# Kernel tuning notes

Hardware: AMD Instinct MI355X
Metric: run time of the kernel (lower is better)

The kernel has to match this reference:

```python
import jax, jax.numpy as jnp
import numpy as np

B, K, N, E, D = 32, 32, 2048, 16384, 768
L_GNN, L_TR, H = 2, 4, 12
FF, VOCAB, N_ROLES, MAX_POS, N_HOPS = 3072, 25, 2, 64, 16


def setup_inputs() -> dict:
    key = jax.random.key(0)
    ks = jax.random.split(key, 32)
    s = 0.02
    inp = {
        "raw_features": jax.random.normal(ks[0], (B, K, D), jnp.float32),
        "x0": jax.random.randint(ks[1], (K, N), 0, VOCAB),
        "edge0": jax.random.randint(ks[2], (K, 2, E), 0, N),
        "batch0": jnp.sort(jax.random.randint(ks[3], (K, N), 0, B), axis=-1),
        "x1": jax.random.randint(ks[4], (K, N), 0, VOCAB),
        "edge1": jax.random.randint(ks[5], (K, 2, E), 0, N),
        "batch1": jnp.sort(jax.random.randint(ks[6], (K, N), 0, B), axis=-1),
        "role_ids": jax.random.randint(ks[7], (B, K), 0, N_ROLES),
        "position_ids": jax.random.randint(ks[8], (B, K), 0, MAX_POS),
        "hop_ids": jax.random.randint(ks[9], (B, K), 0, N_HOPS),
        # GNNForProtein params (shared across slots and both proteins)
        "amino_embed": jax.random.normal(ks[10], (VOCAB, D)) * s,
        "gnn_W": jax.random.normal(ks[11], (L_GNN, D, D)) * s,
        "gnn_b": jnp.zeros((L_GNN, D)),
        # GraphBert embeddings
        "role_emb": jax.random.normal(ks[12], (N_ROLES, D)) * s,
        "pos_emb": jax.random.normal(ks[13], (MAX_POS, D)) * s,
        "hop_emb": jax.random.normal(ks[14], (N_HOPS, D)) * s,
        "emb_ln_scale": jnp.ones((D,)),
        "emb_ln_bias": jnp.zeros((D,)),
        # GraphBert transformer layers (stacked over L_TR)
        "Wq": jax.random.normal(ks[15], (L_TR, D, D)) * s,
        "bq": jnp.zeros((L_TR, D)),
        "Wk": jax.random.normal(ks[16], (L_TR, D, D)) * s,
        "bk": jnp.zeros((L_TR, D)),
        "Wv": jax.random.normal(ks[17], (L_TR, D, D)) * s,
        "bv": jnp.zeros((L_TR, D)),
        "Wo": jax.random.normal(ks[18], (L_TR, D, D)) * s,
        "bo": jnp.zeros((L_TR, D)),
        "ln1_s": jnp.ones((L_TR, D)),
        "ln1_b": jnp.zeros((L_TR, D)),
        "W1": jax.random.normal(ks[19], (L_TR, D, FF)) * s,
        "b1": jnp.zeros((L_TR, FF)),
        "W2": jax.random.normal(ks[20], (L_TR, FF, D)) * s,
        "b2": jnp.zeros((L_TR, D)),
        "ln2_s": jnp.ones((L_TR, D)),
        "ln2_b": jnp.zeros((L_TR, D)),
    }
    return inp


def _ln(x, s, b):
    m = jnp.mean(x, -1, keepdims=True)
    v = jnp.mean(jnp.square(x - m), -1, keepdims=True)
    return (x - m) * jax.lax.rsqrt(v + 1e-12) * s + b


def _gnn(node_ids, edges, batch_idx, amino_embed, W, b):
    # One protein slot: GCN message passing + mean readout per graph in batch.
    h = amino_embed[node_ids]                      # [N, D]
    src, dst = edges[0], edges[1]
    for l in range(W.shape[0]):
        agg = jax.ops.segment_sum(h[src], dst, num_segments=N)
        h = jax.nn.relu((h + agg) @ W[l] + b[l])
    sums = jax.ops.segment_sum(h, batch_idx, num_segments=B)
    cnt = jax.ops.segment_sum(jnp.ones((h.shape[0], 1), h.dtype), batch_idx, num_segments=B)
    return sums / jnp.maximum(cnt, 1.0)           # [B, D]


def reference(raw_features, x0, edge0, batch0, x1, edge1, batch1, role_ids, position_ids, hop_ids,
              amino_embed, gnn_W, gnn_b, role_emb, pos_emb, hop_emb, emb_ln_scale, emb_ln_bias,
              Wq, bq, Wk, bk, Wv, bv, Wo, bo, ln1_s, ln1_b, W1, b1, W2, b2, ln2_s, ln2_b):
    # vmap over the K protein slots replaces the original Python loop (same math).
    gnn_v = jax.vmap(_gnn, in_axes=(0, 0, 0, None, None, None))
    p0 = gnn_v(x0, edge0, batch0, amino_embed, gnn_W, gnn_b)   # [K, B, D]
    p1 = gnn_v(x1, edge1, batch1, amino_embed, gnn_W, gnn_b)   # [K, B, D]
    feats = raw_features + jnp.transpose(p0 + p1, (1, 0, 2))   # [B, K, D]
    # GraphBert embeddings + encoder
    h = feats + role_emb[role_ids] + pos_emb[position_ids] + hop_emb[hop_ids]
    h = _ln(h, emb_ln_scale, emb_ln_bias)
    dh = D // H
    scale = float(1.0 / np.sqrt(dh))
    for l in range(Wq.shape[0]):
        q = (h @ Wq[l] + bq[l]).reshape(B, K, H, dh)
        kk = (h @ Wk[l] + bk[l]).reshape(B, K, H, dh)
        v = (h @ Wv[l] + bv[l]).reshape(B, K, H, dh)
        att = jax.nn.softmax(jnp.einsum('bqhd,bkhd->bhqk', q, kk) * scale, axis=-1)
        ctx = jnp.einsum('bhqk,bkhd->bqhd', att, v).reshape(B, K, D)
        h = _ln(h + ctx @ Wo[l] + bo[l], ln1_s[l], ln1_b[l])
        f = jax.nn.gelu(h @ W1[l] + b1[l]) @ W2[l] + b2[l]
        h = _ln(h + f, ln2_s[l], ln2_b[l])
    return h
```

## Files before the change

kernel.cpp:

```cpp
#include <hip/hip_runtime.h>
#include <hip/hip_bf16.h>
#include <math.h>

using bf16 = __hip_bfloat16;
typedef __attribute__((ext_vector_type(8))) short short8;
typedef __attribute__((ext_vector_type(4))) float floatx4;
typedef __attribute__((ext_vector_type(4))) short short4v;

#define NB   32
#define NK   32
#define NNODE 2048
#define NEDGE 16384
#define ND   768
#define NHH  12
#define DHH  64
#define NFF  3072
#define NG   64
#define LTR  4
#define VOCAB 25

static __device__ __forceinline__ float b2f(bf16 x) { return __bfloat162float(x); }
static __device__ __forceinline__ bf16 f2b(float x) { return __float2bfloat16(x); }
static __device__ __forceinline__ float bs2f(short s) {
    unsigned u = ((unsigned)(unsigned short)s) << 16;
    float f; __builtin_memcpy(&f, &u, 4); return f;
}
static __device__ __forceinline__ short f2bs(float x) {
    bf16 h = f2b(x); short s; __builtin_memcpy(&s, &h, 2); return s;
}

static __device__ __forceinline__ void load_lds16(const bf16* g, bf16* l) {
    __builtin_amdgcn_global_load_lds((const __attribute__((address_space(1))) void*)g,
                                     (__attribute__((address_space(3))) void*)l, 16, 0, 0);
}

static __device__ __forceinline__ float ldf(const void* p, size_t i, bool f32) {
    return f32 ? ((const float*)p)[i] : b2f(((const bf16*)p)[i]);
}

__global__ void detect_dtype_kernel(const void* __restrict__ eln_s, int* __restrict__ flag) {
    if (threadIdx.x == 0 && blockIdx.x == 0) {
        unsigned w = ((const unsigned*)eln_s)[0];
        flag[0] = (w == 0x3F800000u) ? 1 : 0;
    }
}

__device__ __forceinline__ void conv_tile(const void* __restrict__ src, size_t srcOff,
                                          bf16* __restrict__ dst, int R, int Cn,
                                          int tr, int tc, bool f32, int t,
                                          short (*tile)[70]) {
    int r0 = tr * 64, c0 = tc * 64;
    int rr = t >> 4, c4 = (t & 15) * 4;
    #pragma unroll
    for (int p = 0; p < 4; ++p) {
        int r = rr + p * 16;
        size_t base = srcOff + (size_t)(r0 + r) * Cn + c0 + c4;
        short4v s;
        if (f32) {
            float4 v = *(const float4*)((const float*)src + base);
            s.x = f2bs(v.x); s.y = f2bs(v.y); s.z = f2bs(v.z); s.w = f2bs(v.w);
        } else {
            s = *(const short4v*)((const short*)src + base);
        }
        tile[r][c4]     = s.x; tile[r][c4 + 1] = s.y;
        tile[r][c4 + 2] = s.z; tile[r][c4 + 3] = s.w;
    }
    __syncthreads();
    #pragma unroll
    for (int p = 0; p < 4; ++p) {
        int c = rr + p * 16;
        short4v o;
        o.x = tile[c4][c];     o.y = tile[c4 + 1][c];
        o.z = tile[c4 + 2][c]; o.w = tile[c4 + 3][c];
        *(short4v*)((short*)dst + (size_t)(c0 + c) * R + r0 + c4) = o;
    }
}

__global__ __launch_bounds__(256) void convert_gnn_kernel(const void* __restrict__ gnnW,
                                                          bf16* __restrict__ gnnT,
                                                          const int* __restrict__ flag) {
    __shared__ short tile[64][70];
    bool f32 = flag[0] != 0;
    int bid = blockIdx.x;
    int id = bid / 144, tl = bid % 144;
    conv_tile(gnnW, (size_t)id * 589824, gnnT + (size_t)id * 589824,
              768, 768, tl / 12, tl % 12, f32, threadIdx.x, tile);
}

__global__ __launch_bounds__(256) void convert_layer_kernel(
    const void* __restrict__ Wq, const void* __restrict__ Wk, const void* __restrict__ Wv,
    const void* __restrict__ Wo, const void* __restrict__ W1, const void* __restrict__ W2,
    int l, bf16* __restrict__ qkvT, bf16* __restrict__ oT,
    bf16* __restrict__ w1T, bf16* __restrict__ w2T, const int* __restrict__ flag) {
    __shared__ short tile[64][70];
    bool f32 = flag[0] != 0;
    int bid = blockIdx.x, t = threadIdx.x;
    if (bid < 432) {
        int m = bid / 144, tl = bid % 144;
        const void* src = (m == 0) ? Wq : ((m == 1) ? Wk : Wv);
        conv_tile(src, (size_t)l * 589824, qkvT + (size_t)m * 589824,
                  768, 768, tl / 12, tl % 12, f32, t, tile);
    } else if (bid < 576) {
        int tl = bid - 432;
        conv_tile(Wo, (size_t)l * 589824, oT, 768, 768, tl / 12, tl % 12, f32, t, tile);
    } else if (bid < 1152) {
        int tl = bid - 576;
        conv_tile(W1, (size_t)l * 768 * 3072, w1T, 768, 3072, tl / 48, tl % 48, f32, t, tile);
    } else {
        int tl = bid - 1152;
        conv_tile(W2, (size_t)l * 3072 * 768, w2T, 3072, 768, tl / 12, tl % 12, f32, t, tile);
    }
}

__global__ __launch_bounds__(256) void pack_bias_kernel(
    const void* __restrict__ gnnb, const void* __restrict__ bq, const void* __restrict__ bk,
    const void* __restrict__ bv, const void* __restrict__ bo, const void* __restrict__ b1,
    const void* __restrict__ b2, float* __restrict__ out, const int* __restrict__ flag) {
    bool f32 = flag[0] != 0;
    int i = blockIdx.x * 256 + threadIdx.x;
    if (i >= 1536 + LTR * 6912) return;
    float v;
    if (i < 1536) v = ldf(gnnb, i, f32);
    else {
        int j = i - 1536, l = j / 6912, r = j % 6912;
        if      (r <  768) v = ldf(bq, l * 768 + r, f32);
        else if (r < 1536) v = ldf(bk, l * 768 + r - 768, f32);
        else if (r < 2304) v = ldf(bv, l * 768 + r - 1536, f32);
        else if (r < 3072) v = ldf(bo, l * 768 + r - 2304, f32);
        else if (r < 6144) v = ldf(b1, l * 3072 + r - 3072, f32);
        else               v = ldf(b2, l * 768 + r - 6144, f32);
    }
    out[i] = v;
}

__global__ __launch_bounds__(192) void e1_kernel(const void* __restrict__ emb,
                                                 const bf16* __restrict__ w0T,
                                                 bf16* __restrict__ E1,
                                                 const int* __restrict__ flag) {
    bool f32 = flag[0] != 0;
    int v = blockIdx.x, t = threadIdx.x;
    float acc[4] = {0.f, 0.f, 0.f, 0.f};
    for (int k = 0; k < ND; k += 4) {
        float e0 = ldf(emb, (size_t)v * ND + k,     f32);
        float e1 = ldf(emb, (size_t)v * ND + k + 1, f32);
        float e2 = ldf(emb, (size_t)v * ND + k + 2, f32);
        float e3 = ldf(emb, (size_t)v * ND + k + 3, f32);
        #pragma unroll
        for (int j = 0; j < 4; ++j) {
            const short4v w = *(const short4v*)&w0T[(size_t)(t * 4 + j) * ND + k];
            acc[j] += e0 * bs2f(w.x) + e1 * bs2f(w.y) + e2 * bs2f(w.z) + e3 * bs2f(w.w);
        }
    }
    short4v o; o.x = f2bs(acc[0]); o.y = f2bs(acc[1]); o.z = f2bs(acc[2]); o.w = f2bs(acc[3]);
    ((short4v*)(E1 + (size_t)v * ND))[t] = o;
}

__global__ __launch_bounds__(256) void count_deg_kernel(const int* __restrict__ edge0,
                                                        const int* __restrict__ edge1,
                                                        int* __restrict__ deg) {
    int gid = blockIdx.x;
    int g = gid >> 6, chunk = gid & 63;
    const int* ep = (g < NK) ? (edge0 + (size_t)g * 2 * NEDGE)
                             : (edge1 + (size_t)(g - NK) * 2 * NEDGE);
    int e = chunk * 256 + threadIdx.x;
    int dst = ep[NEDGE + e];
    atomicAdd(&deg[g * NNODE + dst], 1);
}

__global__ __launch_bounds__(256) void scan_deg_kernel(int* __restrict__ deg,
                                                       int* __restrict__ indptr) {
    int g = blockIdx.x, t = threadIdx.x;
    __shared__ int sums[256];
    int loc[8]; int s = 0;
    #pragma unroll
    for (int i = 0; i < 8; ++i) { loc[i] = deg[g * NNODE + t * 8 + i]; s += loc[i]; }
    sums[t] = s; __syncthreads();
    for (int off = 1; off < 256; off <<= 1) {
        int v = (t >= off) ? sums[t - off] : 0;
        __syncthreads();
        sums[t] += v;
        __syncthreads();
    }
    int run = sums[t] - s;
    #pragma unroll
    for (int i = 0; i < 8; ++i) {
        indptr[g * (NNODE + 1) + t * 8 + i] = run;
        deg[g * NNODE + t * 8 + i] = run;
        run += loc[i];
    }
    if (t == 255) indptr[g * (NNODE + 1) + NNODE] = run;
}

__global__ __launch_bounds__(256) void fill_csr_kernel(const int* __restrict__ edge0,
                                                       const int* __restrict__ edge1,
                                                       int* __restrict__ cursor,
                                                       int* __restrict__ csr_src) {
    int gid = blockIdx.x;
    int g = gid >> 6, chunk = gid & 63;
    const int* ep = (g < NK) ? (edge0 + (size_t)g * 2 * NEDGE)
                             : (edge1 + (size_t)(g - NK) * 2 * NEDGE);
    int e = chunk * 256 + threadIdx.x;
    int src = ep[e];
    int dst = ep[NEDGE + e];
    int p = atomicAdd(&cursor[g * NNODE + dst], 1);
    csr_src[(size_t)g * NEDGE + p] = src;
}

__global__ __launch_bounds__(64) void batch_count_kernel(const int* __restrict__ batch0,
                                                         const int* __restrict__ batch1,
                                                         int* __restrict__ cnt) {
    int g = blockIdx.x;
    int b = threadIdx.x;
    if (b >= NB) return;
    const int* bp = (g < NK) ? (batch0 + (size_t)g * NNODE)
                             : (batch1 + (size_t)(g - NK) * NNODE);
    int lo = 0, hi = NNODE;
    while (lo < hi) { int mid = (lo + hi) >> 1; if (bp[mid] < b) lo = mid + 1; else hi = mid; }
    int start = lo;
    hi = NNODE;
    while (lo < hi) { int mid = (lo + hi) >> 1; if (bp[mid] < b + 1) lo = mid + 1; else hi = mid; }
    cnt[g * NB + b] = lo - start;
}

__global__ __launch_bounds__(192) void gnn_layer1_kernel(const int* __restrict__ x0,
                                                         const int* __restrict__ x1,
                                                         const bf16* __restrict__ E1,
                                                         const float* __restrict__ b0,
                                                         const int* __restrict__ indptr,
                                                         const int* __restrict__ csr_src,
                                                         bf16* __restrict__ hC, int g0) {
    int id = blockIdx.x;
    int r = id & 7, q = id >> 3;
    int gl = r + 8 * (q >> 10);
    int np = q & 1023;
    int t = threadIdx.x;
    int j = t / 96, ln = t % 96;
    int n = np * 2 + j;
    int g = g0 + gl;
    const int* xg = (g < NK) ? (x0 + (size_t)g * NNODE) : (x1 + (size_t)(g - NK) * NNODE);
    int beg = indptr[g * (NNODE + 1) + n];
    int end = indptr[g * (NNODE + 1) + n + 1];
    const int* cs = csr_src + (size_t)g * NEDGE;
    const short8* E = (const short8*)E1;
    short8 v = E[(size_t)xg[n] * 96 + ln];
    float a[8];
    #pragma unroll
    for (int u = 0; u < 8; ++u) a[u] = bs2f(v[u]);
    int e = beg;
    for (; e + 3 < end; e += 4) {
        int s1 = cs[e], s2 = cs[e + 1], s3 = cs[e + 2], s4 = cs[e + 3];
        short8 w1 = E[(size_t)xg[s1] * 96 + ln];
        short8 w2 = E[(size_t)xg[s2] * 96 + ln];
        short8 w3 = E[(size_t)xg[s3] * 96 + ln];
        short8 w4 = E[(size_t)xg[s4] * 96 + ln];
        #pragma unroll
        for (int u = 0; u < 8; ++u)
            a[u] += (bs2f(w1[u]) + bs2f(w2[u])) + (bs2f(w3[u]) + bs2f(w4[u]));
    }
    for (; e < end; ++e) {
        short8 w = E[(size_t)xg[cs[e]] * 96 + ln];
        #pragma unroll
        for (int u = 0; u < 8; ++u) a[u] += bs2f(w[u]);
    }
    float4 ba = ((const float4*)b0)[ln * 2];
    float4 bb = ((const float4*)b0)[ln * 2 + 1];
    short8 o;
    o[0] = f2bs(fmaxf(a[0] + ba.x, 0.f)); o[1] = f2bs(fmaxf(a[1] + ba.y, 0.f));
    o[2] = f2bs(fmaxf(a[2] + ba.z, 0.f)); o[3] = f2bs(fmaxf(a[3] + ba.w, 0.f));
    o[4] = f2bs(fmaxf(a[4] + bb.x, 0.f)); o[5] = f2bs(fmaxf(a[5] + bb.y, 0.f));
    o[6] = f2bs(fmaxf(a[6] + bb.z, 0.f)); o[7] = f2bs(fmaxf(a[7] + bb.w, 0.f));
    ((short8*)(hC + ((size_t)gl * NNODE + n) * ND))[ln] = o;
}

__global__ __launch_bounds__(192) void gnn_aggregate_kernel(const bf16* __restrict__ hC,
                                                            const int* __restrict__ indptr,
                                                            const int* __restrict__ csr_src,
                                                            bf16* __restrict__ xC, int g0) {
    int id = blockIdx.x;
    int r = id & 7, q = id >> 3;
    int gl = r + 8 * (q >> 10);
    int np = q & 1023;
    int t = threadIdx.x;
    int j = t / 96, ln = t % 96;
    int n = np * 2 + j;
    int g = g0 + gl;
    int beg = indptr[g * (NNODE + 1) + n];
    int end = indptr[g * (NNODE + 1) + n + 1];
    const short8* hg = (const short8*)(hC + (size_t)gl * NNODE * ND);
    const int* cs = csr_src + (size_t)g * NEDGE;
    short8 v = hg[(size_t)n * 96 + ln];
    float a[8];
    #pragma unroll
    for (int u = 0; u < 8; ++u) a[u] = bs2f(v[u]);
    int e = beg;
    for (; e + 3 < end; e += 4) {
        int s1 = cs[e], s2 = cs[e + 1], s3 = cs[e + 2], s4 = cs[e + 3];
        short8 w1 = hg[(size_t)s1 * 96 + ln];
        short8 w2 = hg[(size_t)s2 * 96 + ln];
        short8 w3 = hg[(size_t)s3 * 96 + ln];
        short8 w4 = hg[(size_t)s4 * 96 + ln];
        #pragma unroll
        for (int u = 0; u < 8; ++u)
            a[u] += (bs2f(w1[u]) + bs2f(w2[u])) + (bs2f(w3[u]) + bs2f(w4[u]));
    }
    for (; e < end; ++e) {
        short8 w = hg[(size_t)cs[e] * 96 + ln];
        #pragma unroll
        for (int u = 0; u < 8; ++u) a[u] += bs2f(w[u]);
    }
    short8 o;
    #pragma unroll
    for (int u = 0; u < 8; ++u) o[u] = f2bs(a[u]);
    ((short8*)(xC + ((size_t)gl * NNODE + n) * ND))[ln] = o;
}

__global__ __launch_bounds__(512) void gemm8_pool(const bf16* __restrict__ A,
                                                  const bf16* __restrict__ BT,
                                                  const float* __restrict__ bias,
                                                  int M, int K, int N,
                                                  const int* __restrict__ batAp,
                                                  const int* __restrict__ batBp,
                                                  float* __restrict__ pool, int g0) {
    __shared__ bf16 sA[3][256][64];
    __shared__ bf16 sB[2][128][64];
    const int nt = K >> 6;
    int nTN = N >> 7;
    int xcd = blockIdx.x & 7, jb = blockIdx.x >> 3;
    int brow = (jb / nTN) * 8 + xcd;
    int bcol = jb % nTN;
    const int row0 = brow << 8, col0 = bcol << 7;
    int t = threadIdx.x;
    int wid = t >> 6, lane = t & 63;
    int wr = wid >> 1, wc = wid & 1;
    int l15 = lane & 15, kx = lane >> 4, sw = lane & 7;

    const bf16* Abase = A + (size_t)row0 * K;
    const bf16* Bbase = BT + (size_t)col0 * K;

    auto stage = [&](const bf16* g, bf16* slot, int r0) {
        int r = r0 + (t >> 3);
        int ks = ((t & 7) ^ ((t >> 3) & 7)) << 3;
        load_lds16(g + (size_t)r * K + ks, slot + ((size_t)r0 << 6) + ((size_t)t << 3));
    };
    auto rdA = [&](int s, int i, int kh) {
        return *(const short8*)&sA[s][wr * 64 + i * 16 + l15][(((kh << 2) | kx) ^ sw) << 3];
    };
    auto rdB = [&](int s, int j, int kh) {
        return *(const short8*)&sB[s][wc * 64 + j * 16 + l15][(((kh << 2) | kx) ^ sw) << 3];
    };

    stage(Abase, &sA[0][0][0], 0);   stage(Abase, &sA[0][0][0], 64);
    stage(Abase, &sA[0][0][0], 128); stage(Abase, &sA[0][0][0], 192);
    stage(Bbase, &sB[0][0][0], 0);   stage(Bbase, &sB[0][0][0], 64);
    const bf16* gA1 = Abase + 64;
    stage(gA1, &sA[1][0][0], 0);   stage(gA1, &sA[1][0][0], 64);
    stage(gA1, &sA[1][0][0], 128); stage(gA1, &sA[1][0][0], 192);
    asm volatile("s_waitcnt vmcnt(4)" ::: "memory");
    __builtin_amdgcn_s_barrier();

    floatx4 acc[4][4] = {};
    for (int kt = 0; kt < nt; ++kt) {
        int sa = kt % 3, sb = kt & 1;
        bf16* saN = &sA[(kt + 2) % 3][0][0];
        const bf16* gA = Abase + (kt + 2) * 64;
        short8 af[4], bf[4];
        #pragma unroll
        for (int i = 0; i < 4; ++i) af[i] = rdA(sa, i, 0);
        #pragma unroll
        for (int j = 0; j < 4; ++j) bf[j] = rdB(sb, j, 0);
        if (kt + 1 < nt) {
            const bf16* gB = Bbase + (kt + 1) * 64;
            bf16* sbN = &sB[(kt + 1) & 1][0][0];
            stage(gB, sbN, 0); stage(gB, sbN, 64);
        }
        if (kt + 2 < nt) { stage(gA, saN, 0); stage(gA, saN, 64); }
        __builtin_amdgcn_s_barrier();
        asm volatile("s_waitcnt lgkmcnt(0)" ::: "memory");
        __builtin_amdgcn_s_setprio(1);
        #pragma unroll
        for (int i = 0; i < 4; ++i)
            #pragma unroll
            for (int j = 0; j < 4; ++j)
                acc[i][j] = __builtin_amdgcn_mfma_f32_16x16x32_bf16(af[i], bf[j], acc[i][j], 0, 0, 0);
        __builtin_amdgcn_s_setprio(0);
        __builtin_amdgcn_s_barrier();
        #pragma unroll
        for (int i = 0; i < 4; ++i) af[i] = rdA(sa, i, 1);
        #pragma unroll
        for (int j = 0; j < 4; ++j) bf[j] = rdB(sb, j, 1);
        if (kt + 2 < nt) { stage(gA, saN, 128); stage(gA, saN, 192); }
        __builtin_amdgcn_s_barrier();
        asm volatile("s_waitcnt lgkmcnt(0)" ::: "memory");
        __builtin_amdgcn_s_setprio(1);
        #pragma unroll
        for (int i = 0; i < 4; ++i)
            #pragma unroll
            for (int j = 0; j < 4; ++j)
                acc[i][j] = __builtin_amdgcn_mfma_f32_16x16x32_bf16(af[i], bf[j], acc[i][j], 0, 0, 0);
        __builtin_amdgcn_s_setprio(0);
        if (kt + 1 < nt) {
            if (kt + 2 < nt) asm volatile("s_waitcnt vmcnt(4)" ::: "memory");
            else             asm volatile("s_waitcnt vmcnt(0)" ::: "memory");
            __builtin_amdgcn_s_barrier();
        }
    }

    __syncthreads();
    int g = g0 + (row0 >> 11);
    const int* bp = (g < NK) ? (batAp + (size_t)g * NNODE)
                             : (batBp + (size_t)(g - NK) * NNODE);
    int nbase = row0 & (NNODE - 1);
    float* pg = pool + (size_t)g * NB * ND;
    int cb = wc * 64 + l15;
    float bv[4];
    #pragma unroll
    for (int j = 0; j < 4; ++j) bv[j] = bias[col0 + cb + j * 16];
    float* lp = (float*)sA;
    int bLo = bp[nbase], bHi = bp[nbase + 255];
    int nb = (bHi - bLo + 1) * 128;
    for (int idx = t; idx < nb; idx += 512) lp[idx] = 0.f;
    __syncthreads();
    float sums[4] = {0.f, 0.f, 0.f, 0.f};
    int curb = -1;
    #pragma unroll
    for (int i = 0; i < 4; ++i) {
        int rr = nbase + wr * 64 + i * 16 + kx * 4;
        #pragma unroll
        for (int r = 0; r < 4; ++r) {
            int b = bp[rr + r];
            if (b != curb) {
                if (curb >= 0) {
                    #pragma unroll
                    for (int j = 0; j < 4; ++j)
                        atomicAdd(&lp[(curb - bLo) * 128 + cb + j * 16], sums[j]);
                }
                curb = b;
                sums[0] = sums[1] = sums[2] = sums[3] = 0.f;
            }
            #pragma unroll
            for (int j = 0; j < 4; ++j)
                sums[j] += fmaxf(acc[i][j][r] + bv[j], 0.f);
        }
    }
    #pragma unroll
    for (int j = 0; j < 4; ++j)
        atomicAdd(&lp[(curb - bLo) * 128 + cb + j * 16], sums[j]);
    __syncthreads();
    for (int idx = t; idx < nb; idx += 512) {
        float v = lp[idx];
        if (v != 0.f)
            atomicAdd(&pg[(size_t)(bLo + (idx >> 7)) * ND + col0 + (idx & 127)], v);
    }
}

__global__ __launch_bounds__(256) void gemm_tn_sk(const bf16* __restrict__ A,
                                                  const bf16* __restrict__ BT,
                                                  const float* __restrict__ bias,
                                                  void* __restrict__ C,
                                                  int M, int K, int N, int splitK,
                                                  int act, int store) {
    __shared__ bf16 lA[2][64][64];
    __shared__ bf16 lB[2][128][64];
    int nTN = N >> 7, nTM = M >> 6;
    int tiles = nTM * nTN;
    int split = blockIdx.x / tiles;
    int jt = blockIdx.x % tiles;
    int brow = jt / nTN, bcol = jt % nTN;
    int t = threadIdx.x;
    int wave = t >> 6, lane = t & 63;
    int wr = wave >> 1, wc = wave & 1;
    int l15 = lane & 15, kx = lane >> 4, sw = lane & 7;
    const int row0 = brow << 6, col0 = bcol << 7;
    const int kLen = K / splitK, kBeg = split * kLen;
    const int nt = kLen >> 6;
    const bf16* Abase = A + (size_t)row0 * K + kBeg;
    const bf16* Bbase = BT + (size_t)col0 * K + kBeg;

    auto stage = [&](const bf16* gsrc, bf16* slot, int r0) {
        int rr = r0 + (t >> 3);
        int ks = ((t & 7) ^ (rr & 7)) << 3;
        load_lds16(gsrc + (size_t)rr * K + ks, slot + ((size_t)r0 << 6) + ((size_t)t << 3));
    };
    auto stageTile = [&](int kt, int buf) {
        const bf16* gA = Abase + kt * 64;
        const bf16* gB = Bbase + kt * 64;
        stage(gA, &lA[buf][0][0], 0);  stage(gA, &lA[buf][0][0], 32);
        stage(gB, &lB[buf][0][0], 0);  stage(gB, &lB[buf][0][0], 32);
        stage(gB, &lB[buf][0][0], 64); stage(gB, &lB[buf][0][0], 96);
    };
    auto rdA = [&](int s, int i, int kh) {
        return *(const short8*)&lA[s][wr * 32 + i * 16 + l15][(((kh << 2) | kx) ^ sw) << 3];
    };
    auto rdB = [&](int s, int jj, int kh) {
        return *(const short8*)&lB[s][wc * 64 + jj * 16 + l15][(((kh << 2) | kx) ^ sw) << 3];
    };

    stageTile(0, 0);
    __syncthreads();

    floatx4 acc[2][4] = {};
    int cur = 0;
    for (int kt = 0; kt < nt; ++kt) {
        if (kt + 1 < nt) stageTile(kt + 1, cur ^ 1);
        #pragma unroll
        for (int kh = 0; kh < 2; ++kh) {
            short8 af[2], bf2[4];
            #pragma unroll
            for (int i = 0; i < 2; ++i) af[i] = rdA(cur, i, kh);
            #pragma unroll
            for (int jj = 0; jj < 4; ++jj) bf2[jj] = rdB(cur, jj, kh);
            #pragma unroll
            for (int i = 0; i < 2; ++i)
                #pragma unroll
                for (int jj = 0; jj < 4; ++jj)
                    acc[i][jj] = __builtin_amdgcn_mfma_f32_16x16x32_bf16(af[i], bf2[jj], acc[i][jj], 0, 0, 0);
        }
        __syncthreads();
        cur ^= 1;
    }
    #pragma unroll
    for (int i = 0; i < 2; ++i) {
        int rbase = row0 + wr * 32 + i * 16 + kx * 4;
        #pragma unroll
        for (int j = 0; j < 4; ++j) {
            int c = col0 + wc * 64 + j * 16 + l15;
            float bv = (split == 0) ? bias[c] : 0.f;
            #pragma unroll
            for (int r = 0; r < 4; ++r) {
                float v = acc[i][j][r] + bv;
                if (act == 1) v = fmaxf(v, 0.f);
                else if (act == 2) {
                    float x = v;
                    float u = 1.5957691216057308f * (x + 0.044715f * x * x * x);
                    v = x / (1.f + __expf(-u));
                }
                size_t idx = (size_t)(rbase + r) * N + c;
                if (store == 0)      atomicAdd(&((float*)C)[idx], v);
                else if (store == 1) ((float*)C)[idx] = v;
                else                 ((bf16*)C)[idx] = f2b(v);
            }
        }
    }
}

__device__ __forceinline__ float block_sum_768(float v, int t, float* red) {
    #pragma unroll
    for (int off = 32; off > 0; off >>= 1) v += __shfl_xor(v, off);
    if ((t & 63) == 0) red[t >> 6] = v;
    __syncthreads();
    float s = red[0] + red[1] + red[2] + red[3];
    __syncthreads();
    return s;
}

__device__ __forceinline__ void block_ln_768(float (&x)[3], int t,
                                             const void* __restrict__ s,
                                             const void* __restrict__ b,
                                             size_t sOff, bool f32,
                                             float (&y)[3], float* red) {
    float mean = block_sum_768(x[0] + x[1] + x[2], t, red) * (1.f / 768.f);
    float vs = 0.f;
    #pragma unroll
    for (int e = 0; e < 3; ++e) { float d = x[e] - mean; vs += d * d; }
    float var = block_sum_768(vs, t, red) * (1.f / 768.f);
    float inv = rsqrtf(var + 1e-12f);
    #pragma unroll
    for (int e = 0; e < 3; ++e) {
        int d = t + e * 256;
        y[e] = (x[e] - mean) * inv * ldf(s, sOff + d, f32) + ldf(b, sOff + d, f32);
    }
}

__global__ __launch_bounds__(256) void combine_embed_ln_kernel(
    const void* __restrict__ raw, const float* __restrict__ pooled,
    const int* __restrict__ cnt,
    const int* __restrict__ role_ids, const int* __restrict__ pos_ids, const int* __restrict__ hop_ids,
    const void* __restrict__ role_emb, const void* __restrict__ pos_emb, const void* __restrict__ hop_emb,
    const void* __restrict__ lns, const void* __restrict__ lnb,
    float* __restrict__ hT, bf16* __restrict__ hbf,
    const int* __restrict__ flag) {
    bool f32 = flag[0] != 0;
    __shared__ float red[8];
    int token = blockIdx.x;
    int b = token >> 5, k = token & 31;
    int t = threadIdx.x;
    int rid = role_ids[b * NK + k];
    int pid = pos_ids[b * NK + k];
    int hid = hop_ids[b * NK + k];
    float inv0 = 1.f / (float)max(cnt[k * NB + b], 1);
    float inv1 = 1.f / (float)max(cnt[(NK + k) * NB + b], 1);
    float x[3], y[3];
    #pragma unroll
    for (int e = 0; e < 3; ++e) {
        int d = t + e * 256;
        float p0 = pooled[((size_t)k * NB + b) * ND + d] * inv0;
        float p1 = pooled[((size_t)(NK + k) * NB + b) * ND + d] * inv1;
        x[e] = ldf(raw, (size_t)token * ND + d, f32) + p0 + p1
             + ldf(role_emb, (size_t)rid * ND + d, f32)
             + ldf(pos_emb, (size_t)pid * ND + d, f32)
             + ldf(hop_emb, (size_t)hid * ND + d, f32);
    }
    block_ln_768(x, t, lns, lnb, 0, f32, y, red);
    #pragma unroll
    for (int e = 0; e < 3; ++e) {
        int d = t + e * 256;
        hT[(size_t)token * ND + d] = y[e];
        hbf[(size_t)token * ND + d] = f2b(y[e]);
    }
}

__global__ __launch_bounds__(256) void add_ln_kernel(float* __restrict__ hT,
                                                     const void* __restrict__ lns,
                                                     const void* __restrict__ lnb,
                                                     unsigned long long sOff,
                                                     void* __restrict__ outp, int extOut,
                                                     const int* __restrict__ flag) {
    bool f32 = flag[0] != 0;
    __shared__ float red[8];
    int token = blockIdx.x;
    int t = threadIdx.x;
    float x[3], y[3];
    #pragma unroll
    for (int e = 0; e < 3; ++e) {
        int d = t + e * 256;
        x[e] = hT[(size_t)token * ND + d];
    }
    block_ln_768(x, t, lns, lnb, sOff, f32, y, red);
    #pragma unroll
    for (int e = 0; e < 3; ++e) {
        int d = t + e * 256;
        size_t idx = (size_t)token * ND + d;
        hT[idx] = y[e];
        if (extOut && f32) ((float*)outp)[idx] = y[e];
        else               ((bf16*)outp)[idx] = f2b(y[e]);
    }
}

__global__ __launch_bounds__(256) void attn_kernel(const bf16* __restrict__ qkv,
                                                   bf16* __restrict__ ctx) {
    int blk = blockIdx.x;
    int b = blk / NHH, h = blk % NHH;
    __shared__ float lq[NK][DHH], lk[NK][DHH], lv[NK][DHH];
    __shared__ float ls[NK][NK];
    int t = threadIdx.x;
    {
        int tok = t >> 3, d8 = (t & 7) * 8;
        size_t base = ((size_t)(b * NK + tok)) * (3 * ND) + h * DHH + d8;
        short8 q8 = *(const short8*)&qkv[base];
        short8 k8 = *(const short8*)&qkv[base + ND];
        short8 v8 = *(const short8*)&qkv[base + 2 * ND];
        #pragma unroll
        for (int j = 0; j < 8; ++j) {
            lq[tok][d8 + j] = bs2f(q8[j]);
            lk[tok][d8 + j] = bs2f(k8[j]);
            lv[tok][d8 + j] = bs2f(v8[j]);
        }
    }
    __syncthreads();
    const float scale = 0.125f;
    for (int i = t; i < NK * NK; i += 256) {
        int qi = i >> 5, kj = i & 31;
        float s = 0.f;
        #pragma unroll
        for (int d = 0; d < DHH; ++d) s += lq[qi][d] * lk[kj][d];
        ls[qi][kj] = s * scale;
    }
    __syncthreads();
    if (t < NK) {
        float m = -1e30f;
        for (int j = 0; j < NK; ++j) m = fmaxf(m, ls[t][j]);
        float sum = 0.f;
        for (int j = 0; j < NK; ++j) { float e = expf(ls[t][j] - m); ls[t][j] = e; sum += e; }
        float inv = 1.f / sum;
        for (int j = 0; j < NK; ++j) ls[t][j] *= inv;
    }
    __syncthreads();
    for (int i = t; i < NK * DHH; i += 256) {
        int qi = i >> 6, d = i & 63;
        float s = 0.f;
        #pragma unroll
        for (int j = 0; j < NK; ++j) s += ls[qi][j] * lv[j][d];
        ctx[((size_t)(b * NK + qi)) * ND + h * DHH + d] = f2b(s);
    }
}

extern "C" void kernel_launch(void* const* d_in, const int* in_sizes, int n_in,
                              void* d_out, int out_size, void* d_ws, size_t ws_size,
                              hipStream_t stream) {
    const void* raw      = d_in[0];
    const int*  x0       = (const int*)d_in[1];
    const int*  edge0    = (const int*)d_in[2];
    const int*  batch0   = (const int*)d_in[3];
    const int*  x1       = (const int*)d_in[4];
    const int*  edge1    = (const int*)d_in[5];
    const int*  batch1   = (const int*)d_in[6];
    const int*  role_ids = (const int*)d_in[7];
    const int*  pos_ids  = (const int*)d_in[8];
    const int*  hop_ids  = (const int*)d_in[9];
    const void* amino    = d_in[10];
    const void* gnnW     = d_in[11];
    const void* gnnb     = d_in[12];
    const void* role_emb = d_in[13];
    const void* pos_emb  = d_in[14];
    const void* hop_emb  = d_in[15];
    const void* eln_s    = d_in[16];
    const void* eln_b    = d_in[17];
    const void* Wq       = d_in[18];
    const void* bq       = d_in[19];
    const void* Wk       = d_in[20];
    const void* bk       = d_in[21];
    const void* Wv       = d_in[22];
    const void* bv       = d_in[23];
    const void* Wo       = d_in[24];
    const void* bo       = d_in[25];
    const void* ln1_s    = d_in[26];
    const void* ln1_b    = d_in[27];
    const void* W1       = d_in[28];
    const void* b1       = d_in[29];
    const void* W2       = d_in[30];
    const void* b2       = d_in[31];
    const void* ln2_s    = d_in[32];
    const void* ln2_b    = d_in[33];

    char* ws = (char*)d_ws;
    size_t off = 0;
    auto alloc = [&](size_t bytes) -> void* {
        void* p = ws + off;
        off = (off + bytes + 255) & ~(size_t)255;
        return p;
    };
    int*   dflag   = (int*)alloc(256);
    float* pooled  = (float*)alloc((size_t)NG * NB * ND * 4);
    int*   cntb    = (int*)alloc((size_t)NG * NB * 4);
    int*   indptr  = (int*)alloc((size_t)NG * (NNODE + 1) * 4);
    int*   csr_src = (int*)alloc((size_t)NG * NEDGE * 4);
    int*   degcur  = (int*)alloc((size_t)NG * NNODE * 4);
    bf16*  gnnT    = (bf16*)alloc((size_t)2 * ND * ND * 2);
    bf16*  E1      = (bf16*)alloc((size_t)VOCAB * ND * 2);
    float* biasPk  = (float*)alloc((size_t)(1536 + LTR * 6912) * 4);
    const size_t QS = (size_t)3 * ND * ND, OS = (size_t)ND * ND;
    const size_t S1 = (size_t)ND * NFF,    S2 = (size_t)NFF * ND;
    bf16*  qkvT    = (bf16*)alloc(QS * 2);
    bf16*  oT      = (bf16*)alloc(OS * 2);
    bf16*  w1T     = (bf16*)alloc(S1 * 2);
    bf16*  w2T     = (bf16*)alloc(S2 * 2);

    const size_t perG  = (size_t)NNODE * ND * 2;
    const size_t bigTR = 21 * 1024 * 1024;
    int gc = 8;
    for (int cand = 32; cand >= 8; cand >>= 1) {
        size_t bigGNN = 2 * (size_t)cand * perG;
        size_t need = off + (bigGNN > bigTR ? bigGNN : bigTR) + (1 << 20);
        if (need <= ws_size) { gc = cand; break; }
    }
    char* bigbase = (char*)alloc(2 * (size_t)gc * perG > bigTR ? 2 * (size_t)gc * perG : bigTR);
    bf16* hC = (bf16*)bigbase;
    bf16* xC = (bf16*)(bigbase + (size_t)gc * perG);
    size_t toff = 0;
    auto talloc = [&](size_t bytes) -> void* {
        void* p = bigbase + toff;
        toff = (toff + bytes + 255) & ~(size_t)255;
        return p;
    };
    float* hT    = (float*)talloc((size_t)NB * NK * ND * 4);
    bf16*  hbf   = (bf16*)talloc((size_t)NB * NK * ND * 2);
    bf16*  qkvb  = (bf16*)talloc((size_t)NB * NK * 3 * ND * 2);
    bf16*  ctxb  = (bf16*)talloc((size_t)NB * NK * ND * 2);
    bf16*  ffbuf = (bf16*)talloc((size_t)NB * NK * NFF * 2);

    auto gemm_sk = [&](const bf16* A, const bf16* BT, const float* bias, void* C,
                       int Mm, int Kk, int Nn, int splitK, int act, int store) {
        int blocks = (Mm >> 6) * (Nn >> 7) * splitK;
        gemm_tn_sk<<<blocks, 256, 0, stream>>>(A, BT, bias, C, Mm, Kk, Nn, splitK, act, store);
    };

    detect_dtype_kernel<<<1, 64, 0, stream>>>(eln_s, dflag);

    convert_gnn_kernel<<<288, 256, 0, stream>>>(gnnW, gnnT, dflag);
    pack_bias_kernel<<<(1536 + LTR * 6912 + 255) / 256, 256, 0, stream>>>(
        gnnb, bq, bk, bv, bo, b1, b2, biasPk, dflag);
    e1_kernel<<<VOCAB, 192, 0, stream>>>(amino, gnnT, E1, dflag);

    hipMemsetAsync(degcur, 0, (size_t)NG * NNODE * 4, stream);
    hipMemsetAsync(pooled, 0, (size_t)NG * NB * ND * 4, stream);
    count_deg_kernel<<<NG * 64, 256, 0, stream>>>(edge0, edge1, degcur);
    scan_deg_kernel<<<NG, 256, 0, stream>>>(degcur, indptr);
    fill_csr_kernel<<<NG * 64, 256, 0, stream>>>(edge0, edge1, degcur, csr_src);
    batch_count_kernel<<<NG, 64, 0, stream>>>(batch0, batch1, cntb);

    for (int g0 = 0; g0 < NG; g0 += gc) {
        gnn_layer1_kernel<<<gc * (NNODE / 2), 192, 0, stream>>>(x0, x1, E1, biasPk,
                                                                indptr, csr_src, hC, g0);
        gnn_aggregate_kernel<<<gc * (NNODE / 2), 192, 0, stream>>>(hC, indptr, csr_src, xC, g0);
        int blocks = ((gc * NNODE) >> 8) * (ND >> 7);
        gemm8_pool<<<blocks, 512, 0, stream>>>(xC, gnnT + (size_t)ND * ND, biasPk + ND,
                                               gc * NNODE, ND, ND,
                                               batch0, batch1, pooled, g0);
    }

    combine_embed_ln_kernel<<<NB * NK, 256, 0, stream>>>(
        raw, pooled, cntb, role_ids, pos_ids, hop_ids,
        role_emb, pos_emb, hop_emb, eln_s, eln_b, hT, hbf, dflag);

    const int M = NB * NK;
    for (int l = 0; l < LTR; ++l) {
        convert_layer_kernel<<<1728, 256, 0, stream>>>(Wq, Wk, Wv, Wo, W1, W2, l,
                                                       qkvT, oT, w1T, w2T, dflag);
        const float* lb = biasPk + 1536 + l * 6912;
        gemm_sk(hbf, qkvT, lb, qkvb, M, ND, 3 * ND, 1, 0, 2);
        attn_kernel<<<NB * NHH, 256, 0, stream>>>(qkvb, ctxb);
        gemm_sk(ctxb, oT, lb + 2304, hT, M, ND, ND, 2, 0, 0);
        add_ln_kernel<<<M, 256, 0, stream>>>(hT, ln1_s, ln1_b,
                                             (unsigned long long)l * ND, hbf, 0, dflag);
        gemm_sk(hbf, w1T, lb + 3072, ffbuf, M, ND, NFF, 1, 2, 2);
        gemm_sk(ffbuf, w2T, lb + 6144, hT, M, NFF, ND, 4, 0, 0);
        int ext = (l == LTR - 1) ? 1 : 0;
        void* outb = ext ? d_out : (void*)hbf;
        add_ln_kernel<<<M, 256, 0, stream>>>(hT, ln2_s, ln2_b,
                                             (unsigned long long)l * ND, outb, ext, dflag);
    }
}
```

Baseline: 1.257 ms.

## Batch weight conversion, vectorize CSR build, read first GNN weight directly

Converts all four transformer layers' weights in one launch when workspace allows, replacing four per-layer conversion launches. The first GNN layer's embedding projection now reads the original weights directly, so only the second GNN weight gets transposed. Degree counting and CSR fill each process four edges per thread with vector loads, and workspace selection now prefers a larger GNN chunk size (64 graphs per pass). The Wo GEMM split-K changes from 2 to 3, and the upfront conversion uses more workspace memory.

After: 1.364 ms. 8.5% more time.

```diff
diff --git a/kernel.cpp b/kernel.cpp
--- a/kernel.cpp
+++ b/kernel.cpp
@@ -81,20 +81,16 @@
                                                           const int* __restrict__ flag) {
     __shared__ short tile[64][70];
     bool f32 = flag[0] != 0;
-    int bid = blockIdx.x;
-    int id = bid / 144, tl = bid % 144;
-    conv_tile(gnnW, (size_t)id * 589824, gnnT + (size_t)id * 589824,
+    int tl = blockIdx.x;
+    conv_tile(gnnW, (size_t)589824, gnnT,
               768, 768, tl / 12, tl % 12, f32, threadIdx.x, tile);
 }
 
-__global__ __launch_bounds__(256) void convert_layer_kernel(
-    const void* __restrict__ Wq, const void* __restrict__ Wk, const void* __restrict__ Wv,
-    const void* __restrict__ Wo, const void* __restrict__ W1, const void* __restrict__ W2,
-    int l, bf16* __restrict__ qkvT, bf16* __restrict__ oT,
-    bf16* __restrict__ w1T, bf16* __restrict__ w2T, const int* __restrict__ flag) {
-    __shared__ short tile[64][70];
-    bool f32 = flag[0] != 0;
-    int bid = blockIdx.x, t = threadIdx.x;
+__device__ __forceinline__ void conv_layer_body(
+    const void* Wq, const void* Wk, const void* Wv, const void* Wo,
+    const void* W1, const void* W2, int l,
+    bf16* qkvT, bf16* oT, bf16* w1T, bf16* w2T,
+    bool f32, int bid, int t, short (*tile)[70]) {
     if (bid < 432) {
         int m = bid / 144, tl = bid % 144;
         const void* src = (m == 0) ? Wq : ((m == 1) ? Wk : Wv);
@@ -110,6 +106,29 @@
         int tl = bid - 1152;
         conv_tile(W2, (size_t)l * 3072 * 768, w2T, 3072, 768, tl / 12, tl % 12, f32, t, tile);
     }
+}
+
+__global__ __launch_bounds__(256) void convert_layer_kernel(
+    const void* __restrict__ Wq, const void* __restrict__ Wk, const void* __restrict__ Wv,
+    const void* __restrict__ Wo, const void* __restrict__ W1, const void* __restrict__ W2,
+    int l, bf16* __restrict__ qkvT, bf16* __restrict__ oT,
+    bf16* __restrict__ w1T, bf16* __restrict__ w2T, const int* __restrict__ flag) {
+    __shared__ short tile[64][70];
+    conv_layer_body(Wq, Wk, Wv, Wo, W1, W2, l, qkvT, oT, w1T, w2T,
+                    flag[0] != 0, blockIdx.x, threadIdx.x, tile);
+}
+
+__global__ __launch_bounds__(256) void convert_layers_all(
+    const void* __restrict__ Wq, const void* __restrict__ Wk, const void* __restrict__ Wv,
+    const void* __restrict__ Wo, const void* __restrict__ W1, const void* __restrict__ W2,
+    bf16* __restrict__ qkvT, bf16* __restrict__ oT,
+    bf16* __restrict__ w1T, bf16* __restrict__ w2T, const int* __restrict__ flag) {
+    __shared__ short tile[64][70];
+    int l = blockIdx.x / 1728, bid = blockIdx.x % 1728;
+    conv_layer_body(Wq, Wk, Wv, Wo, W1, W2, l,
+                    qkvT + (size_t)l * 3 * ND * ND, oT + (size_t)l * ND * ND,
+                    w1T + (size_t)l * ND * NFF, w2T + (size_t)l * NFF * ND,
+                    flag[0] != 0, bid, threadIdx.x, tile);
 }
 
 __global__ __launch_bounds__(256) void pack_bias_kernel(
@@ -134,21 +153,21 @@
 }
 
 __global__ __launch_bounds__(192) void e1_kernel(const void* __restrict__ emb,
-                                                 const bf16* __restrict__ w0T,
+                                                 const void* __restrict__ gnnW,
                                                  bf16* __restrict__ E1,
                                                  const int* __restrict__ flag) {
     bool f32 = flag[0] != 0;
     int v = blockIdx.x, t = threadIdx.x;
     float acc[4] = {0.f, 0.f, 0.f, 0.f};
-    for (int k = 0; k < ND; k += 4) {
-        float e0 = ldf(emb, (size_t)v * ND + k,     f32);
-        float e1 = ldf(emb, (size_t)v * ND + k + 1, f32);
-        float e2 = ldf(emb, (size_t)v * ND + k + 2, f32);
-        float e3 = ldf(emb, (size_t)v * ND + k + 3, f32);
-        #pragma unroll
-        for (int j = 0; j < 4; ++j) {
-            const short4v w = *(const short4v*)&w0T[(size_t)(t * 4 + j) * ND + k];
-            acc[j] += e0 * bs2f(w.x) + e1 * bs2f(w.y) + e2 * bs2f(w.z) + e3 * bs2f(w.w);
+    for (int k = 0; k < ND; ++k) {
+        float e = ldf(emb, (size_t)v * ND + k, f32);
+        if (f32) {
+            float4 w = *(const float4*)((const float*)gnnW + (size_t)k * ND + t * 4);
+            acc[0] += e * w.x; acc[1] += e * w.y; acc[2] += e * w.z; acc[3] += e * w.w;
+        } else {
+            short4v w = *(const short4v*)((const short*)gnnW + (size_t)k * ND + t * 4);
+            acc[0] += e * bs2f(w.x); acc[1] += e * bs2f(w.y);
+            acc[2] += e * bs2f(w.z); acc[3] += e * bs2f(w.w);
         }
     }
     short4v o; o.x = f2bs(acc[0]); o.y = f2bs(acc[1]); o.z = f2bs(acc[2]); o.w = f2bs(acc[3]);
@@ -159,12 +178,15 @@
                                                         const int* __restrict__ edge1,
                                                         int* __restrict__ deg) {
     int gid = blockIdx.x;
-    int g = gid >> 6, chunk = gid & 63;
+    int g = gid >> 4, chunk = gid & 15;
     const int* ep = (g < NK) ? (edge0 + (size_t)g * 2 * NEDGE)
                              : (edge1 + (size_t)(g - NK) * 2 * NEDGE);
-    int e = chunk * 256 + threadIdx.x;
-    int dst = ep[NEDGE + e];
-    atomicAdd(&deg[g * NNODE + dst], 1);
+    int base = (chunk * 256 + threadIdx.x) * 4;
+    int4 d = *(const int4*)&ep[NEDGE + base];
+    atomicAdd(&deg[g * NNODE + d.x], 1);
+    atomicAdd(&deg[g * NNODE + d.y], 1);
+    atomicAdd(&deg[g * NNODE + d.z], 1);
+    atomicAdd(&deg[g * NNODE + d.w], 1);
 }
 
 __global__ __launch_bounds__(256) void scan_deg_kernel(int* __restrict__ deg,
@@ -196,14 +218,19 @@
                                                        int* __restrict__ cursor,
                                                        int* __restrict__ csr_src) {
     int gid = blockIdx.x;
-    int g = gid >> 6, chunk = gid & 63;
+    int g = gid >> 4, chunk = gid & 15;
     const int* ep = (g < NK) ? (edge0 + (size_t)g * 2 * NEDGE)
                              : (edge1 + (size_t)(g - NK) * 2 * NEDGE);
-    int e = chunk * 256 + threadIdx.x;
-    int src = ep[e];
-    int dst = ep[NEDGE + e];
-    int p = atomicAdd(&cursor[g * NNODE + dst], 1);
-    csr_src[(size_t)g * NEDGE + p] = src;
+    int base = (chunk * 256 + threadIdx.x) * 4;
+    int4 sv = *(const int4*)&ep[base];
+    int4 dv = *(const int4*)&ep[NEDGE + base];
+    int* cur = cursor + g * NNODE;
+    int* cg = (int*)(csr_src + (size_t)g * NEDGE);
+    int p;
+    p = atomicAdd(&cur[dv.x], 1); cg[p] = sv.x;
+    p = atomicAdd(&cur[dv.y], 1); cg[p] = sv.y;
+    p = atomicAdd(&cur[dv.z], 1); cg[p] = sv.z;
+    p = atomicAdd(&cur[dv.w], 1); cg[p] = sv.w;
 }
 
 __global__ __launch_bounds__(64) void batch_count_kernel(const int* __restrict__ batch0,
@@ -735,24 +762,31 @@
     int*   indptr  = (int*)alloc((size_t)NG * (NNODE + 1) * 4);
     int*   csr_src = (int*)alloc((size_t)NG * NEDGE * 4);
     int*   degcur  = (int*)alloc((size_t)NG * NNODE * 4);
-    bf16*  gnnT    = (bf16*)alloc((size_t)2 * ND * ND * 2);
+    bf16*  gnnT    = (bf16*)alloc((size_t)ND * ND * 2);
     bf16*  E1      = (bf16*)alloc((size_t)VOCAB * ND * 2);
     float* biasPk  = (float*)alloc((size_t)(1536 + LTR * 6912) * 4);
     const size_t QS = (size_t)3 * ND * ND, OS = (size_t)ND * ND;
     const size_t S1 = (size_t)ND * NFF,    S2 = (size_t)NFF * ND;
-    bf16*  qkvT    = (bf16*)alloc(QS * 2);
-    bf16*  oT      = (bf16*)alloc(OS * 2);
-    bf16*  w1T     = (bf16*)alloc(S1 * 2);
-    bf16*  w2T     = (bf16*)alloc(S2 * 2);
+    const size_t wPerLayer = (QS + OS + S1 + S2) * 2;
 
     const size_t perG  = (size_t)NNODE * ND * 2;
     const size_t bigTR = 21 * 1024 * 1024;
-    int gc = 8;
-    for (int cand = 32; cand >= 8; cand >>= 1) {
-        size_t bigGNN = 2 * (size_t)cand * perG;
-        size_t need = off + (bigGNN > bigTR ? bigGNN : bigTR) + (1 << 20);
-        if (need <= ws_size) { gc = cand; break; }
-    }
+    int gc = 8, nlw = 1;
+    {
+        const int cands[6][2] = {{64, 4}, {64, 1}, {32, 4}, {32, 1}, {16, 1}, {8, 1}};
+        for (int i = 0; i < 6; ++i) {
+            size_t bigGNN = 2 * (size_t)cands[i][0] * perG;
+            size_t big = bigGNN > bigTR ? bigGNN : bigTR;
+            if (off + (size_t)cands[i][1] * wPerLayer + big + (1 << 20) <= ws_size) {
+                gc = cands[i][0]; nlw = cands[i][1]; break;
+            }
+        }
+    }
+    bf16* qkvT = (bf16*)alloc(QS * 2 * nlw);
+    bf16* oT   = (bf16*)alloc(OS * 2 * nlw);
+    bf16* w1T  = (bf16*)alloc(S1 * 2 * nlw);
+    bf16* w2T  = (bf16*)alloc(S2 * 2 * nlw);
+
     char* bigbase = (char*)alloc(2 * (size_t)gc * perG > bigTR ? 2 * (size_t)gc * perG : bigTR);
     bf16* hC = (bf16*)bigbase;
     bf16* xC = (bf16*)(bigbase + (size_t)gc * perG);
@@ -776,16 +810,19 @@
 
     detect_dtype_kernel<<<1, 64, 0, stream>>>(eln_s, dflag);
 
-    convert_gnn_kernel<<<288, 256, 0, stream>>>(gnnW, gnnT, dflag);
+    convert_gnn_kernel<<<144, 256, 0, stream>>>(gnnW, gnnT, dflag);
     pack_bias_kernel<<<(1536 + LTR * 6912 + 255) / 256, 256, 0, stream>>>(
         gnnb, bq, bk, bv, bo, b1, b2, biasPk, dflag);
-    e1_kernel<<<VOCAB, 192, 0, stream>>>(amino, gnnT, E1, dflag);
+    e1_kernel<<<VOCAB, 192, 0, stream>>>(amino, gnnW, E1, dflag);
+    if (nlw == 4)
+        convert_layers_all<<<4 * 1728, 256, 0, stream>>>(Wq, Wk, Wv, Wo, W1, W2,
+                                                         qkvT, oT, w1T, w2T, dflag);
 
     hipMemsetAsync(degcur, 0, (size_t)NG * NNODE * 4, stream);
     hipMemsetAsync(pooled, 0, (size_t)NG * NB * ND * 4, stream);
-    count_deg_kernel<<<NG * 64, 256, 0, stream>>>(edge0, edge1, degcur);
+    count_deg_kernel<<<NG * 16, 256, 0, stream>>>(edge0, edge1, degcur);
     scan_deg_kernel<<<NG, 256, 0, stream>>>(degcur, indptr);
-    fill_csr_kernel<<<NG * 64, 256, 0, stream>>>(edge0, edge1, degcur, csr_src);
+    fill_csr_kernel<<<NG * 16, 256, 0, stream>>>(edge0, edge1, degcur, csr_src);
     batch_count_kernel<<<NG, 64, 0, stream>>>(batch0, batch1, cntb);
 
     for (int g0 = 0; g0 < NG; g0 += gc) {
@@ -793,7 +830,7 @@
                                                                 indptr, csr_src, hC, g0);
         gnn_aggregate_kernel<<<gc * (NNODE / 2), 192, 0, stream>>>(hC, indptr, csr_src, xC, g0);
         int blocks = ((gc * NNODE) >> 8) * (ND >> 7);
-        gemm8_pool<<<blocks, 512, 0, stream>>>(xC, gnnT + (size_t)ND * ND, biasPk + ND,
+        gemm8_pool<<<blocks, 512, 0, stream>>>(xC, gnnT, biasPk + ND,
                                                gc * NNODE, ND, ND,
                                                batch0, batch1, pooled, g0);
     }
@@ -804,16 +841,21 @@
 
     const int M = NB * NK;
     for (int l = 0; l < LTR; ++l) {
-        convert_layer_kernel<<<1728, 256, 0, stream>>>(Wq, Wk, Wv, Wo, W1, W2, l,
-                                                       qkvT, oT, w1T, w2T, dflag);
+        bf16* qkvTl = qkvT + (size_t)(nlw == 4 ? l : 0) * QS;
+        bf16* oTl   = oT   + (size_t)(nlw == 4 ? l : 0) * OS;
+        bf16* w1Tl  = w1T  + (size_t)(nlw == 4 ? l : 0) * S1;
+        bf16* w2Tl  = w2T  + (size_t)(nlw == 4 ? l : 0) * S2;
+        if (nlw == 1)
+            convert_layer_kernel<<<1728, 256, 0, stream>>>(Wq, Wk, Wv, Wo, W1, W2, l,
+                                                           qkvTl, oTl, w1Tl, w2Tl, dflag);
         const float* lb = biasPk + 1536 + l * 6912;
-        gemm_sk(hbf, qkvT, lb, qkvb, M, ND, 3 * ND, 1, 0, 2);
+        gemm_sk(hbf, qkvTl, lb, qkvb, M, ND, 3 * ND, 1, 0, 2);
         attn_kernel<<<NB * NHH, 256, 0, stream>>>(qkvb, ctxb);
-        gemm_sk(ctxb, oT, lb + 2304, hT, M, ND, ND, 2, 0, 0);
+        gemm_sk(ctxb, oTl, lb + 2304, hT, M, ND, ND, 3, 0, 0);
         add_ln_kernel<<<M, 256, 0, stream>>>(hT, ln1_s, ln1_b,
                                              (unsigned long long)l * ND, hbf, 0, dflag);
-        gemm_sk(hbf, w1T, lb + 3072, ffbuf, M, ND, NFF, 1, 2, 2);
-        gemm_sk(ffbuf, w2T, lb + 6144, hT, M, NFF, ND, 4, 0, 0);
+        gemm_sk(hbf, w1Tl, lb + 3072, ffbuf, M, ND, NFF, 1, 2, 2);
+        gemm_sk(ffbuf, w2Tl, lb + 6144, hT, M, NFF, ND, 4, 0, 0);
         int ext = (l == LTR - 1) ? 1 : 0;
         void* outb = ext ? d_out : (void*)hbf;
         add_ln_kernel<<<M, 256, 0, stream>>>(hT, ln2_s, ln2_b,
```
